# Kernel optimization log

Hardware: AMD Instinct MI355X
Metric: run time of the kernel (lower is better)

Reference implementation:

```python
import jax, jax.numpy as jnp
import numpy as np

N, D, K, R_DIM = 20000, 256, 16, 64
RADIUS = 50.0     # init radius
ALPHA = 2.0       # hardcoded in forward
THRESH = 0.01     # attention_threshold
EPS_LN = 1e-5     # torch LayerNorm default eps


def layer_norm(v, g, b):
    m = jnp.mean(v, axis=-1, keepdims=True)
    var = jnp.mean((v - m) ** 2, axis=-1, keepdims=True)
    return (v - m) / jnp.sqrt(var + EPS_LN) * g + b


def setup_inputs() -> dict:
    key = jax.random.key(0)
    ks = jax.random.split(key, 8)
    x = jax.random.normal(ks[0], (N, D), dtype=jnp.float32)
    # fixed-degree graph: node i has exactly K neighbors
    row = jnp.repeat(jnp.arange(N, dtype=jnp.int32), K)
    col = jax.random.randint(ks[1], (N * K,), 0, N, dtype=jnp.int32)
    edge_index = jnp.stack([row, col], axis=0)
    spatial_coords = jax.random.uniform(ks[2], (N, 2), dtype=jnp.float32) * 100.0
    gamma = jnp.ones((D,), jnp.float32)
    beta_ln = jnp.zeros((D,), jnp.float32)
    W_self = jax.random.normal(ks[3], (D, D), jnp.float32) * 0.05
    b_self = jnp.zeros((D,), jnp.float32)
    W_nei = jax.random.normal(ks[4], (D, D), jnp.float32) * 0.05
    b_nei = jnp.zeros((D,), jnp.float32)
    W_red = jax.random.normal(ks[5], (R_DIM, D), jnp.float32) * 0.05
    b_red = jnp.zeros((R_DIM,), jnp.float32)
    beta_mix = jnp.asarray(0.5, jnp.float32)
    return {"x": x, "spatial_coords": spatial_coords, "gamma": gamma,
            "beta_ln": beta_ln, "W_self": W_self, "b_self": b_self,
            "W_nei": W_nei, "b_nei": b_nei, "W_red": W_red, "b_red": b_red,
            "beta_mix": beta_mix, "edge_index": edge_index}


def reference(x, spatial_coords, gamma, beta_ln, W_self, b_self, W_nei, b_nei,
              W_red, b_red, beta_mix, edge_index):
    col = edge_index[1].reshape(N, K)              # fixed degree K per node
    neighbors = x[col]                             # [N, K, D] gather
    nb_coords = spatial_coords[col]                # [N, K, 2]
    distances = jnp.linalg.norm(spatial_coords[:, None, :] - nb_coords, axis=-1)  # [N, K]

    t = layer_norm(x, gamma, beta_ln)              # [N, D]
    nb = layer_norm(neighbors, gamma, beta_ln)     # [N, K, D]

    s_scores = t @ W_self.T + b_self               # [N, D]
    n_scores = nb @ W_nei.T + b_nei                # [N, K, D]

    dist_w = jnp.exp(-ALPHA * distances / (RADIUS + 1e-8))  # [N, K]
    weighted_n = n_scores * dist_w[..., None]

    combined = jnp.concatenate([s_scores[:, None, :], weighted_n], axis=1)  # [N, K+1, D]
    cw = jax.nn.softmax(combined, axis=1)
    self_w = cw[:, 0, :]
    nb_w = cw[:, 1:, :]
    self_w = jnp.where(jnp.abs(self_w) >= THRESH, self_w, 0.0)
    nb_w = jnp.where(jnp.abs(nb_w) >= THRESH, nb_w, 0.0)

    context = beta_mix * (self_w * t) + (1.0 - beta_mix) * jnp.sum(nb_w * nb, axis=1)
    reduced = jax.nn.leaky_relu(context @ W_red.T + b_red, 0.01)
    # outer forward applies leaky_relu again (dropout is identity in eval)
    return jax.nn.leaky_relu(reduced, 0.01)
```

## Files before the change

kernel.cpp:

```cpp
#include <hip/hip_runtime.h>
#include <cmath>

#define NN 20000
#define DD 256
#define KK 16
#define LDC3 768

typedef __attribute__((ext_vector_type(8))) short short8;
typedef __attribute__((ext_vector_type(4))) float f32x4;
typedef unsigned int u32;
typedef unsigned short bfu;

__device__ __forceinline__ float b2f(bfu u) {
  union { u32 i; float f; } v; v.i = ((u32)u) << 16; return v.f;
}
__device__ __forceinline__ bfu f2b(float f) {
  u32 u = __float_as_uint(f);
  u = (u + 0x7fff + ((u >> 16) & 1)) >> 16;
  return (bfu)u;
}
__device__ __forceinline__ float wave_sum(float v) {
#pragma unroll
  for (int m = 32; m; m >>= 1) v += __shfl_xor(v, m, 64);
  return v;
}
__device__ __forceinline__ void gl_lds16(const void* g, void* l) {
  __builtin_amdgcn_global_load_lds((const __attribute__((address_space(1))) u32*)g,
                                   (__attribute__((address_space(3))) u32*)l, 16, 0, 0);
}

__global__ __launch_bounds__(256) void prep_kernel(
    const float* __restrict__ x, const float* __restrict__ g,
    const float* __restrict__ b, const float* __restrict__ Wself,
    const float* __restrict__ Wnei, const float* __restrict__ Wred,
    bfu* __restrict__ C3, bfu* __restrict__ Wcat, bfu* __restrict__ Wredb) {
  int bid = blockIdx.x;
  if (bid < 5000) {
    int lane = threadIdx.x & 63;
    int row = (bid << 2) + (threadIdx.x >> 6);
    float4 v = ((const float4*)(x + (size_t)row * DD))[lane];
    float mean = wave_sum(v.x + v.y + v.z + v.w) * (1.0f / 256.0f);
    float4 d = make_float4(v.x - mean, v.y - mean, v.z - mean, v.w - mean);
    float var = wave_sum(d.x * d.x + d.y * d.y + d.z * d.z + d.w * d.w) * (1.0f / 256.0f);
    float rstd = 1.0f / sqrtf(var + 1e-5f);
    float4 g4 = ((const float4*)g)[lane];
    float4 b4 = ((const float4*)b)[lane];
    ushort4 ov;
    ov.x = f2b(d.x * rstd * g4.x + b4.x);
    ov.y = f2b(d.y * rstd * g4.y + b4.y);
    ov.z = f2b(d.z * rstd * g4.z + b4.z);
    ov.w = f2b(d.w * rstd * g4.w + b4.w);
    *(ushort4*)(C3 + (size_t)row * LDC3 + 512 + (lane << 2)) = ov;
  } else {
    int idx = (bid - 5000) * 256 + threadIdx.x;
    if (idx < 65536) Wcat[idx] = f2b(Wself[idx]);
    else if (idx < 131072) Wcat[idx] = f2b(Wnei[idx - 65536]);
    else if (idx < 147456) Wredb[idx - 131072] = f2b(Wred[idx - 131072]);
  }
}

template<int NT, bool FINAL>
__global__ __launch_bounds__(256) void gemm_kernel(
    const bfu* __restrict__ A, int lda, const bfu* __restrict__ Bw,
    const float* __restrict__ bias0, const float* __restrict__ bias1,
    void* __restrict__ Cout, int ldc, int M) {
  constexpr int FM = (NT == 128) ? 4 : 2;
  constexpr int WM = (NT == 128) ? 64 : 32;
  constexpr int AIT = 4;
  constexpr int BIT = NT / 32;
  __shared__ bfu smA[2][128 * 64];
  __shared__ bfu smB[2][NT * 64];
  int tid = threadIdx.x, lane = tid & 63, wid = tid >> 6;
  int m0 = blockIdx.x * 128;
  int nbase = blockIdx.y * NT;
  const bfu* Bt = Bw + (size_t)nbase * 256;
  int wr = (NT == 128) ? (wid >> 1) : wid;
  int wc = (NT == 128) ? (wid & 1) : 0;
  int lr = lane & 15, lk = lane >> 4;

  f32x4 acc[FM][4];
#pragma unroll
  for (int i = 0; i < FM; ++i)
#pragma unroll
    for (int j = 0; j < 4; ++j) acc[i][j] = (f32x4){0.f, 0.f, 0.f, 0.f};

#define STAGE(buf, kc)                                                          \
  {                                                                             \
    _Pragma("unroll") for (int i = 0; i < AIT; ++i) {                           \
      int p = tid + 256 * i; int row = p >> 3; int c = (p & 7) ^ (row & 7);     \
      gl_lds16(A + (size_t)(m0 + row) * lda + (kc) + c * 8, &smA[buf][p * 8]);  \
    }                                                                           \
    _Pragma("unroll") for (int i = 0; i < BIT; ++i) {                           \
      int p = tid + 256 * i; int row = p >> 3; int c = (p & 7) ^ (row & 7);     \
      gl_lds16(Bt + (size_t)row * 256 + (kc) + c * 8, &smB[buf][p * 8]);        \
    }                                                                           \
  }

#define COMPUTE(buf)                                                            \
  {                                                                             \
    _Pragma("unroll") for (int h = 0; h < 2; ++h) {                             \
      short8 af[FM], bfr[4];                                                    \
      int cc = h * 4 + lk;                                                      \
      _Pragma("unroll") for (int fm = 0; fm < FM; ++fm) {                       \
        int row = wr * WM + fm * 16 + lr;                                       \
        af[fm] = *(const short8*)&smA[buf][row * 64 + ((cc ^ (row & 7)) << 3)]; \
      }                                                                         \
      _Pragma("unroll") for (int fn = 0; fn < 4; ++fn) {                        \
        int row = wc * 64 + fn * 16 + lr;                                       \
        bfr[fn] = *(const short8*)&smB[buf][row * 64 + ((cc ^ (row & 7)) << 3)];\
      }                                                                         \
      _Pragma("unroll") for (int fm = 0; fm < FM; ++fm)                         \
        _Pragma("unroll") for (int fn = 0; fn < 4; ++fn)                        \
          acc[fm][fn] = __builtin_amdgcn_mfma_f32_16x16x32_bf16(                \
              bfr[fn], af[fm], acc[fm][fn], 0, 0, 0);                           \
    }                                                                           \
  }

  STAGE(0, 0);
  __syncthreads();
  STAGE(1, 64);
  COMPUTE(0);
  __syncthreads();
  STAGE(0, 128);
  COMPUTE(1);
  __syncthreads();
  STAGE(1, 192);
  COMPUTE(0);
  __syncthreads();
  COMPUTE(1);
#undef STAGE
#undef COMPUTE

  const float* bias = (nbase < 256) ? (bias0 + nbase) : (bias1 + (nbase - 256));
#pragma unroll
  for (int fm = 0; fm < FM; ++fm) {
    int m = m0 + wr * WM + fm * 16 + lr;
    if (m >= M) continue;
#pragma unroll
    for (int fn = 0; fn < 4; ++fn) {
      int lc = wc * 64 + fn * 16 + lk * 4;
      float4 bv = *(const float4*)(bias + lc);
      float o0 = acc[fm][fn][0] + bv.x;
      float o1 = acc[fm][fn][1] + bv.y;
      float o2 = acc[fm][fn][2] + bv.z;
      float o3 = acc[fm][fn][3] + bv.w;
      if (FINAL) {
        o0 = (o0 > 0.f) ? o0 : 0.01f * o0; o0 = (o0 > 0.f) ? o0 : 0.01f * o0;
        o1 = (o1 > 0.f) ? o1 : 0.01f * o1; o1 = (o1 > 0.f) ? o1 : 0.01f * o1;
        o2 = (o2 > 0.f) ? o2 : 0.01f * o2; o2 = (o2 > 0.f) ? o2 : 0.01f * o2;
        o3 = (o3 > 0.f) ? o3 : 0.01f * o3; o3 = (o3 > 0.f) ? o3 : 0.01f * o3;
        *(float4*)((float*)Cout + (size_t)m * ldc + nbase + lc) =
            make_float4(o0, o1, o2, o3);
      } else {
        ushort4 ov; ov.x = f2b(o0); ov.y = f2b(o1); ov.z = f2b(o2); ov.w = f2b(o3);
        *(ushort4*)((bfu*)Cout + (size_t)m * ldc + nbase + lc) = ov;
      }
    }
  }
}

__global__ __launch_bounds__(256) void gather_kernel(
    const bfu* __restrict__ C3, const float* __restrict__ coords,
    const int* __restrict__ col, const float* __restrict__ bmix,
    bfu* __restrict__ ctx) {
  const float L2E = 1.4426950408889634f;
  int lane = threadIdx.x & 63;
  int i = (blockIdx.x << 2) + (threadIdx.x >> 6);
  float beta = bmix[0];

  int ck = col[i * KK + (lane & 15)];
  float2 ci = ((const float2*)coords)[i];
  float2 cn = ((const float2*)coords)[ck];
  float dx = ci.x - cn.x, dy = ci.y - cn.y;
  float dwv = exp2f((-2.0f * L2E / (50.0f + 1e-8f)) * sqrtf(dx * dx + dy * dy)) * L2E;

  int d = lane << 2;
  const bfu* rowi = C3 + (size_t)i * LDC3;
  ushort4 sv = *(const ushort4*)(rowi + d);
  float4 e0 = make_float4(exp2f(L2E * b2f(sv.x)), exp2f(L2E * b2f(sv.y)),
                          exp2f(L2E * b2f(sv.z)), exp2f(L2E * b2f(sv.w)));
  float4 Z = e0;
  float4 ef[KK];
  ushort4 tn[KK];
#pragma unroll
  for (int k = 0; k < KK; ++k) {
    int cc = __shfl(ck, k, 64);
    float w = __shfl(dwv, k, 64);
    const bfu* rowc = C3 + (size_t)cc * LDC3;
    ushort4 uv = *(const ushort4*)(rowc + 256 + d);
    tn[k] = *(const ushort4*)(rowc + 512 + d);
    float4 e = make_float4(exp2f(w * b2f(uv.x)), exp2f(w * b2f(uv.y)),
                           exp2f(w * b2f(uv.z)), exp2f(w * b2f(uv.w)));
    ef[k] = e;
    Z.x += e.x; Z.y += e.y; Z.z += e.z; Z.w += e.w;
  }
  float4 thr = make_float4(0.01f * Z.x, 0.01f * Z.y, 0.01f * Z.z, 0.01f * Z.w);
  ushort4 tv = *(const ushort4*)(rowi + 512 + d);
  float ob = 1.0f - beta;
  float4 ns = make_float4(0.f, 0.f, 0.f, 0.f);
#pragma unroll
  for (int k = 0; k < KK; ++k) {
    float ex = (ef[k].x >= thr.x) ? ef[k].x : 0.f;
    float ey = (ef[k].y >= thr.y) ? ef[k].y : 0.f;
    float ez = (ef[k].z >= thr.z) ? ef[k].z : 0.f;
    float ew = (ef[k].w >= thr.w) ? ef[k].w : 0.f;
    ns.x += ex * b2f(tn[k].x); ns.y += ey * b2f(tn[k].y);
    ns.z += ez * b2f(tn[k].z); ns.w += ew * b2f(tn[k].w);
  }
  float s0x = (e0.x >= thr.x) ? e0.x : 0.f;
  float s0y = (e0.y >= thr.y) ? e0.y : 0.f;
  float s0z = (e0.z >= thr.z) ? e0.z : 0.f;
  float s0w = (e0.w >= thr.w) ? e0.w : 0.f;
  ushort4 ov;
  ov.x = f2b((beta * s0x * b2f(tv.x) + ob * ns.x) / Z.x);
  ov.y = f2b((beta * s0y * b2f(tv.y) + ob * ns.y) / Z.y);
  ov.z = f2b((beta * s0z * b2f(tv.z) + ob * ns.z) / Z.z);
  ov.w = f2b((beta * s0w * b2f(tv.w) + ob * ns.w) / Z.w);
  *(ushort4*)(ctx + (size_t)i * DD + d) = ov;
}

extern "C" void kernel_launch(void* const* d_in, const int* in_sizes, int n_in,
                              void* d_out, int out_size, void* d_ws, size_t ws_size,
                              hipStream_t stream) {
  (void)in_sizes; (void)n_in; (void)out_size; (void)ws_size;
  const float* x       = (const float*)d_in[0];
  const float* coords  = (const float*)d_in[1];
  const float* gamma   = (const float*)d_in[2];
  const float* beta_ln = (const float*)d_in[3];
  const float* W_self  = (const float*)d_in[4];
  const float* b_self  = (const float*)d_in[5];
  const float* W_nei   = (const float*)d_in[6];
  const float* b_nei   = (const float*)d_in[7];
  const float* W_red   = (const float*)d_in[8];
  const float* b_red   = (const float*)d_in[9];
  const float* bmix    = (const float*)d_in[10];
  const int*   edge    = (const int*)d_in[11];
  const int*   col     = edge + (size_t)NN * KK;

  bfu* C3    = (bfu*)d_ws;
  bfu* ctx   = (bfu*)((char*)d_ws + 30867456);
  bfu* Wcat  = (bfu*)((char*)d_ws + 41156608);
  bfu* Wredb = (bfu*)((char*)d_ws + 41418752);

  prep_kernel<<<5577, 256, 0, stream>>>(x, gamma, beta_ln, W_self, W_nei, W_red,
                                        C3, Wcat, Wredb);
  gemm_kernel<128, false><<<dim3(157, 4), 256, 0, stream>>>(
      C3 + 512, LDC3, Wcat, b_self, b_nei, (void*)C3, LDC3, NN);
  gather_kernel<<<5000, 256, 0, stream>>>(C3, coords, col, bmix, ctx);
  gemm_kernel<64, true><<<dim3(157, 1), 256, 0, stream>>>(
      ctx, DD, Wredb, b_red, b_red, d_out, 64, NN);
}
```

Measured before the change: 159.8 us.

## Interleave neighbor scores with normalized features and tighten GEMM pipeline waits

Widens the workspace row to 1024 bf16 and interleaves each 4-element chunk of neighbor scores with the matching 4 layer-normed values. The gather kernel can then fetch both with a single 16-byte load per neighbor instead of two 8-byte loads from separate regions. The GEMM prefetches two stages up front and uses explicit vmcnt waits with raw barriers instead of __syncthreads, so loads overlap compute. The final GEMM switches to 64x64 tiles, doubling the grid to 313 blocks, at the cost of an extra LN copy write and a larger workspace.

```diff
diff --git a/kernel.cpp b/kernel.cpp
--- a/kernel.cpp
+++ b/kernel.cpp
@@ -4,7 +4,7 @@
 #define NN 20000
 #define DD 256
 #define KK 16
-#define LDC3 768
+#define LDROW 1024
 
 typedef __attribute__((ext_vector_type(8))) short short8;
 typedef __attribute__((ext_vector_type(4))) float f32x4;
@@ -27,6 +27,14 @@
 __device__ __forceinline__ void gl_lds16(const void* g, void* l) {
   __builtin_amdgcn_global_load_lds((const __attribute__((address_space(1))) u32*)g,
                                    (__attribute__((address_space(3))) u32*)l, 16, 0, 0);
+}
+template<int N> __device__ __forceinline__ void wait_vm() {
+  asm volatile("s_waitcnt vmcnt(%0)" :: "i"(N) : "memory");
+}
+__device__ __forceinline__ void bar() {
+  __builtin_amdgcn_sched_barrier(0);
+  __builtin_amdgcn_s_barrier();
+  __builtin_amdgcn_sched_barrier(0);
 }
 
 __global__ __launch_bounds__(256) void prep_kernel(
@@ -50,7 +58,9 @@
     ov.y = f2b(d.y * rstd * g4.y + b4.y);
     ov.z = f2b(d.z * rstd * g4.z + b4.z);
     ov.w = f2b(d.w * rstd * g4.w + b4.w);
-    *(ushort4*)(C3 + (size_t)row * LDC3 + 512 + (lane << 2)) = ov;
+    bfu* rowp = C3 + (size_t)row * LDROW;
+    *(ushort4*)(rowp + 768 + (lane << 2)) = ov;
+    *(ushort4*)(rowp + 256 + (lane << 3) + 4) = ov;
   } else {
     int idx = (bid - 5000) * 256 + threadIdx.x;
     if (idx < 65536) Wcat[idx] = f2b(Wself[idx]);
@@ -59,36 +69,34 @@
   }
 }
 
-template<int NT, bool FINAL>
+template<int MT, int NT, int LDA, bool FINAL>
 __global__ __launch_bounds__(256) void gemm_kernel(
-    const bfu* __restrict__ A, int lda, const bfu* __restrict__ Bw,
+    const bfu* __restrict__ A, const bfu* __restrict__ Bw,
     const float* __restrict__ bias0, const float* __restrict__ bias1,
-    void* __restrict__ Cout, int ldc, int M) {
-  constexpr int FM = (NT == 128) ? 4 : 2;
-  constexpr int WM = (NT == 128) ? 64 : 32;
-  constexpr int AIT = 4;
-  constexpr int BIT = NT / 32;
-  __shared__ bfu smA[2][128 * 64];
+    bfu* __restrict__ C3out, float* __restrict__ Fout, int M) {
+  constexpr int WM = MT / 2, WN = NT / 2, FM = WM / 16, FN = WN / 16;
+  constexpr int AIT = MT * 8 / 256, BIT = NT * 8 / 256;
+  constexpr int VM = (MT + NT) / 32;
+  __shared__ bfu smA[2][MT * 64];
   __shared__ bfu smB[2][NT * 64];
   int tid = threadIdx.x, lane = tid & 63, wid = tid >> 6;
-  int m0 = blockIdx.x * 128;
+  int m0 = blockIdx.x * MT;
   int nbase = blockIdx.y * NT;
   const bfu* Bt = Bw + (size_t)nbase * 256;
-  int wr = (NT == 128) ? (wid >> 1) : wid;
-  int wc = (NT == 128) ? (wid & 1) : 0;
+  int wr = wid >> 1, wc = wid & 1;
   int lr = lane & 15, lk = lane >> 4;
 
-  f32x4 acc[FM][4];
+  f32x4 acc[FM][FN];
 #pragma unroll
   for (int i = 0; i < FM; ++i)
 #pragma unroll
-    for (int j = 0; j < 4; ++j) acc[i][j] = (f32x4){0.f, 0.f, 0.f, 0.f};
+    for (int j = 0; j < FN; ++j) acc[i][j] = (f32x4){0.f, 0.f, 0.f, 0.f};
 
 #define STAGE(buf, kc)                                                          \
   {                                                                             \
     _Pragma("unroll") for (int i = 0; i < AIT; ++i) {                           \
       int p = tid + 256 * i; int row = p >> 3; int c = (p & 7) ^ (row & 7);     \
-      gl_lds16(A + (size_t)(m0 + row) * lda + (kc) + c * 8, &smA[buf][p * 8]);  \
+      gl_lds16(A + (size_t)(m0 + row) * LDA + (kc) + c * 8, &smA[buf][p * 8]);  \
     }                                                                           \
     _Pragma("unroll") for (int i = 0; i < BIT; ++i) {                           \
       int p = tid + 256 * i; int row = p >> 3; int c = (p & 7) ^ (row & 7);     \
@@ -99,34 +107,36 @@
 #define COMPUTE(buf)                                                            \
   {                                                                             \
     _Pragma("unroll") for (int h = 0; h < 2; ++h) {                             \
-      short8 af[FM], bfr[4];                                                    \
+      short8 af[FM], bfr[FN];                                                   \
       int cc = h * 4 + lk;                                                      \
       _Pragma("unroll") for (int fm = 0; fm < FM; ++fm) {                       \
         int row = wr * WM + fm * 16 + lr;                                       \
         af[fm] = *(const short8*)&smA[buf][row * 64 + ((cc ^ (row & 7)) << 3)]; \
       }                                                                         \
-      _Pragma("unroll") for (int fn = 0; fn < 4; ++fn) {                        \
-        int row = wc * 64 + fn * 16 + lr;                                       \
+      _Pragma("unroll") for (int fn = 0; fn < FN; ++fn) {                       \
+        int row = wc * WN + fn * 16 + lr;                                       \
         bfr[fn] = *(const short8*)&smB[buf][row * 64 + ((cc ^ (row & 7)) << 3)];\
       }                                                                         \
       _Pragma("unroll") for (int fm = 0; fm < FM; ++fm)                         \
-        _Pragma("unroll") for (int fn = 0; fn < 4; ++fn)                        \
+        _Pragma("unroll") for (int fn = 0; fn < FN; ++fn)                       \
           acc[fm][fn] = __builtin_amdgcn_mfma_f32_16x16x32_bf16(                \
               bfr[fn], af[fm], acc[fm][fn], 0, 0, 0);                           \
     }                                                                           \
   }
 
   STAGE(0, 0);
-  __syncthreads();
   STAGE(1, 64);
+  wait_vm<VM>(); bar();
   COMPUTE(0);
-  __syncthreads();
+  bar();
   STAGE(0, 128);
+  wait_vm<VM>(); bar();
   COMPUTE(1);
-  __syncthreads();
+  bar();
   STAGE(1, 192);
+  wait_vm<VM>(); bar();
   COMPUTE(0);
-  __syncthreads();
+  wait_vm<0>(); bar();
   COMPUTE(1);
 #undef STAGE
 #undef COMPUTE
@@ -137,8 +147,8 @@
     int m = m0 + wr * WM + fm * 16 + lr;
     if (m >= M) continue;
 #pragma unroll
-    for (int fn = 0; fn < 4; ++fn) {
-      int lc = wc * 64 + fn * 16 + lk * 4;
+    for (int fn = 0; fn < FN; ++fn) {
+      int lc = wc * WN + fn * 16 + lk * 4;
       float4 bv = *(const float4*)(bias + lc);
       float o0 = acc[fm][fn][0] + bv.x;
       float o1 = acc[fm][fn][1] + bv.y;
@@ -149,11 +159,15 @@
         o1 = (o1 > 0.f) ? o1 : 0.01f * o1; o1 = (o1 > 0.f) ? o1 : 0.01f * o1;
         o2 = (o2 > 0.f) ? o2 : 0.01f * o2; o2 = (o2 > 0.f) ? o2 : 0.01f * o2;
         o3 = (o3 > 0.f) ? o3 : 0.01f * o3; o3 = (o3 > 0.f) ? o3 : 0.01f * o3;
-        *(float4*)((float*)Cout + (size_t)m * ldc + nbase + lc) =
-            make_float4(o0, o1, o2, o3);
+        *(float4*)(Fout + (size_t)m * NT + nbase + lc) = make_float4(o0, o1, o2, o3);
       } else {
         ushort4 ov; ov.x = f2b(o0); ov.y = f2b(o1); ov.z = f2b(o2); ov.w = f2b(o3);
-        *(ushort4*)((bfu*)Cout + (size_t)m * ldc + nbase + lc) = ov;
+        if (nbase < 256) {
+          *(ushort4*)(C3out + (size_t)m * LDROW + nbase + lc) = ov;
+        } else {
+          int f = nbase - 256 + lc;
+          *(ushort4*)(C3out + (size_t)m * LDROW + 256 + ((f >> 2) << 3)) = ov;
+        }
       }
     }
   }
@@ -175,8 +189,9 @@
   float dwv = exp2f((-2.0f * L2E / (50.0f + 1e-8f)) * sqrtf(dx * dx + dy * dy)) * L2E;
 
   int d = lane << 2;
-  const bfu* rowi = C3 + (size_t)i * LDC3;
+  const bfu* rowi = C3 + (size_t)i * LDROW;
   ushort4 sv = *(const ushort4*)(rowi + d);
+  short8 self8 = *(const short8*)(rowi + 256 + (lane << 3));
   float4 e0 = make_float4(exp2f(L2E * b2f(sv.x)), exp2f(L2E * b2f(sv.y)),
                           exp2f(L2E * b2f(sv.z)), exp2f(L2E * b2f(sv.w)));
   float4 Z = e0;
@@ -186,16 +201,14 @@
   for (int k = 0; k < KK; ++k) {
     int cc = __shfl(ck, k, 64);
     float w = __shfl(dwv, k, 64);
-    const bfu* rowc = C3 + (size_t)cc * LDC3;
-    ushort4 uv = *(const ushort4*)(rowc + 256 + d);
-    tn[k] = *(const ushort4*)(rowc + 512 + d);
-    float4 e = make_float4(exp2f(w * b2f(uv.x)), exp2f(w * b2f(uv.y)),
-                           exp2f(w * b2f(uv.z)), exp2f(w * b2f(uv.w)));
+    short8 v = *(const short8*)(C3 + (size_t)cc * LDROW + 256 + (lane << 3));
+    tn[k].x = (bfu)v[4]; tn[k].y = (bfu)v[5]; tn[k].z = (bfu)v[6]; tn[k].w = (bfu)v[7];
+    float4 e = make_float4(exp2f(w * b2f((bfu)v[0])), exp2f(w * b2f((bfu)v[1])),
+                           exp2f(w * b2f((bfu)v[2])), exp2f(w * b2f((bfu)v[3])));
     ef[k] = e;
     Z.x += e.x; Z.y += e.y; Z.z += e.z; Z.w += e.w;
   }
   float4 thr = make_float4(0.01f * Z.x, 0.01f * Z.y, 0.01f * Z.z, 0.01f * Z.w);
-  ushort4 tv = *(const ushort4*)(rowi + 512 + d);
   float ob = 1.0f - beta;
   float4 ns = make_float4(0.f, 0.f, 0.f, 0.f);
 #pragma unroll
@@ -212,10 +225,10 @@
   float s0z = (e0.z >= thr.z) ? e0.z : 0.f;
   float s0w = (e0.w >= thr.w) ? e0.w : 0.f;
   ushort4 ov;
-  ov.x = f2b((beta * s0x * b2f(tv.x) + ob * ns.x) / Z.x);
-  ov.y = f2b((beta * s0y * b2f(tv.y) + ob * ns.y) / Z.y);
-  ov.z = f2b((beta * s0z * b2f(tv.z) + ob * ns.z) / Z.z);
-  ov.w = f2b((beta * s0w * b2f(tv.w) + ob * ns.w) / Z.w);
+  ov.x = f2b((beta * s0x * b2f((bfu)self8[4]) + ob * ns.x) / Z.x);
+  ov.y = f2b((beta * s0y * b2f((bfu)self8[5]) + ob * ns.y) / Z.y);
+  ov.z = f2b((beta * s0z * b2f((bfu)self8[6]) + ob * ns.z) / Z.z);
+  ov.w = f2b((beta * s0w * b2f((bfu)self8[7]) + ob * ns.w) / Z.w);
   *(ushort4*)(ctx + (size_t)i * DD + d) = ov;
 }
 
@@ -238,15 +251,15 @@
   const int*   col     = edge + (size_t)NN * KK;
 
   bfu* C3    = (bfu*)d_ws;
-  bfu* ctx   = (bfu*)((char*)d_ws + 30867456);
-  bfu* Wcat  = (bfu*)((char*)d_ws + 41156608);
-  bfu* Wredb = (bfu*)((char*)d_ws + 41418752);
-
-  prep_kernel<<<5577, 256, 0, stream>>>(x, gamma, beta_ln, W_self, W_nei, W_red,
+  bfu* ctx   = (bfu*)((char*)d_ws + 41156608);
+  bfu* Wcat  = (bfu*)((char*)d_ws + 51445760);
+  bfu* Wredb = (bfu*)((char*)d_ws + 51707904);
+
+  prep_kernel<<<5576, 256, 0, stream>>>(x, gamma, beta_ln, W_self, W_nei, W_red,
                                         C3, Wcat, Wredb);
-  gemm_kernel<128, false><<<dim3(157, 4), 256, 0, stream>>>(
-      C3 + 512, LDC3, Wcat, b_self, b_nei, (void*)C3, LDC3, NN);
+  gemm_kernel<128, 128, LDROW, false><<<dim3(157, 4), 256, 0, stream>>>(
+      C3 + 768, Wcat, b_self, b_nei, C3, nullptr, NN);
   gather_kernel<<<5000, 256, 0, stream>>>(C3, coords, col, bmix, ctx);
-  gemm_kernel<64, true><<<dim3(157, 1), 256, 0, stream>>>(
-      ctx, DD, Wredb, b_red, b_red, d_out, 64, NN);
-}
+  gemm_kernel<64, 64, 256, true><<<dim3(313, 1), 256, 0, stream>>>(
+      ctx, Wredb, b_red, b_red, nullptr, (float*)d_out, NN);
+}
```

After: 173.6 us. 1.09x slower.

## Fuse final reduction GEMM into gather kernel and use fast exp2/rcp

Applied to the files above, without the earlier changes.

The final 256->64 projection and double leaky_relu are folded into the gather kernel. Each block stages its 4 context rows in LDS as bf16 and runs a 16x16x32 MFMA per wave against bf16 W_red, writing fp32 output directly. This removes the ctx round trip through global memory and one kernel launch, and the GEMM kernel loses its template. The cost is 12 of 16 MFMA rows doing wasted work on uninitialized LDS, plus an added __syncthreads. exp2f and the division are also swapped for the hardware exp2 and rcp intrinsics, which trades a little precision for fewer instructions.

```diff
diff --git a/kernel.cpp b/kernel.cpp
--- a/kernel.cpp
+++ b/kernel.cpp
@@ -28,6 +28,8 @@
   __builtin_amdgcn_global_load_lds((const __attribute__((address_space(1))) u32*)g,
                                    (__attribute__((address_space(3))) u32*)l, 16, 0, 0);
 }
+__device__ __forceinline__ float fexp2(float x) { return __builtin_amdgcn_exp2f(x); }
+__device__ __forceinline__ float frcp(float x)  { return __builtin_amdgcn_rcpf(x); }
 
 __global__ __launch_bounds__(256) void prep_kernel(
     const float* __restrict__ x, const float* __restrict__ g,
@@ -59,61 +61,55 @@
   }
 }
 
-template<int NT, bool FINAL>
 __global__ __launch_bounds__(256) void gemm_kernel(
-    const bfu* __restrict__ A, int lda, const bfu* __restrict__ Bw,
+    const bfu* __restrict__ A, const bfu* __restrict__ Bw,
     const float* __restrict__ bias0, const float* __restrict__ bias1,
-    void* __restrict__ Cout, int ldc, int M) {
-  constexpr int FM = (NT == 128) ? 4 : 2;
-  constexpr int WM = (NT == 128) ? 64 : 32;
-  constexpr int AIT = 4;
-  constexpr int BIT = NT / 32;
+    bfu* __restrict__ Cout, int M) {
   __shared__ bfu smA[2][128 * 64];
-  __shared__ bfu smB[2][NT * 64];
+  __shared__ bfu smB[2][128 * 64];
   int tid = threadIdx.x, lane = tid & 63, wid = tid >> 6;
   int m0 = blockIdx.x * 128;
-  int nbase = blockIdx.y * NT;
+  int nbase = blockIdx.y * 128;
   const bfu* Bt = Bw + (size_t)nbase * 256;
-  int wr = (NT == 128) ? (wid >> 1) : wid;
-  int wc = (NT == 128) ? (wid & 1) : 0;
+  int wr = wid >> 1, wc = wid & 1;
   int lr = lane & 15, lk = lane >> 4;
 
-  f32x4 acc[FM][4];
-#pragma unroll
-  for (int i = 0; i < FM; ++i)
+  f32x4 acc[4][4];
+#pragma unroll
+  for (int i = 0; i < 4; ++i)
 #pragma unroll
     for (int j = 0; j < 4; ++j) acc[i][j] = (f32x4){0.f, 0.f, 0.f, 0.f};
 
-#define STAGE(buf, kc)                                                          \
-  {                                                                             \
-    _Pragma("unroll") for (int i = 0; i < AIT; ++i) {                           \
-      int p = tid + 256 * i; int row = p >> 3; int c = (p & 7) ^ (row & 7);     \
-      gl_lds16(A + (size_t)(m0 + row) * lda + (kc) + c * 8, &smA[buf][p * 8]);  \
-    }                                                                           \
-    _Pragma("unroll") for (int i = 0; i < BIT; ++i) {                           \
-      int p = tid + 256 * i; int row = p >> 3; int c = (p & 7) ^ (row & 7);     \
-      gl_lds16(Bt + (size_t)row * 256 + (kc) + c * 8, &smB[buf][p * 8]);        \
-    }                                                                           \
-  }
-
-#define COMPUTE(buf)                                                            \
-  {                                                                             \
-    _Pragma("unroll") for (int h = 0; h < 2; ++h) {                             \
-      short8 af[FM], bfr[4];                                                    \
-      int cc = h * 4 + lk;                                                      \
-      _Pragma("unroll") for (int fm = 0; fm < FM; ++fm) {                       \
-        int row = wr * WM + fm * 16 + lr;                                       \
-        af[fm] = *(const short8*)&smA[buf][row * 64 + ((cc ^ (row & 7)) << 3)]; \
-      }                                                                         \
-      _Pragma("unroll") for (int fn = 0; fn < 4; ++fn) {                        \
-        int row = wc * 64 + fn * 16 + lr;                                       \
-        bfr[fn] = *(const short8*)&smB[buf][row * 64 + ((cc ^ (row & 7)) << 3)];\
-      }                                                                         \
-      _Pragma("unroll") for (int fm = 0; fm < FM; ++fm)                         \
-        _Pragma("unroll") for (int fn = 0; fn < 4; ++fn)                        \
-          acc[fm][fn] = __builtin_amdgcn_mfma_f32_16x16x32_bf16(                \
-              bfr[fn], af[fm], acc[fm][fn], 0, 0, 0);                           \
-    }                                                                           \
+#define STAGE(buf, kc)                                                           \
+  {                                                                              \
+    _Pragma("unroll") for (int i = 0; i < 4; ++i) {                              \
+      int p = tid + 256 * i; int row = p >> 3; int c = (p & 7) ^ (row & 7);      \
+      gl_lds16(A + (size_t)(m0 + row) * LDC3 + (kc) + c * 8, &smA[buf][p * 8]);  \
+    }                                                                            \
+    _Pragma("unroll") for (int i = 0; i < 4; ++i) {                              \
+      int p = tid + 256 * i; int row = p >> 3; int c = (p & 7) ^ (row & 7);      \
+      gl_lds16(Bt + (size_t)row * 256 + (kc) + c * 8, &smB[buf][p * 8]);         \
+    }                                                                            \
+  }
+
+#define COMPUTE(buf)                                                             \
+  {                                                                              \
+    _Pragma("unroll") for (int h = 0; h < 2; ++h) {                              \
+      short8 af[4], bfr[4];                                                      \
+      int cc = h * 4 + lk;                                                       \
+      _Pragma("unroll") for (int fm = 0; fm < 4; ++fm) {                         \
+        int row = wr * 64 + fm * 16 + lr;                                        \
+        af[fm] = *(const short8*)&smA[buf][row * 64 + ((cc ^ (row & 7)) << 3)];  \
+      }                                                                          \
+      _Pragma("unroll") for (int fn = 0; fn < 4; ++fn) {                         \
+        int row = wc * 64 + fn * 16 + lr;                                        \
+        bfr[fn] = *(const short8*)&smB[buf][row * 64 + ((cc ^ (row & 7)) << 3)]; \
+      }                                                                          \
+      _Pragma("unroll") for (int fm = 0; fm < 4; ++fm)                           \
+        _Pragma("unroll") for (int fn = 0; fn < 4; ++fn)                         \
+          acc[fm][fn] = __builtin_amdgcn_mfma_f32_16x16x32_bf16(                 \
+              bfr[fn], af[fm], acc[fm][fn], 0, 0, 0);                            \
+    }                                                                            \
   }
 
   STAGE(0, 0);
@@ -133,28 +129,19 @@
 
   const float* bias = (nbase < 256) ? (bias0 + nbase) : (bias1 + (nbase - 256));
 #pragma unroll
-  for (int fm = 0; fm < FM; ++fm) {
-    int m = m0 + wr * WM + fm * 16 + lr;
+  for (int fm = 0; fm < 4; ++fm) {
+    int m = m0 + wr * 64 + fm * 16 + lr;
     if (m >= M) continue;
 #pragma unroll
     for (int fn = 0; fn < 4; ++fn) {
       int lc = wc * 64 + fn * 16 + lk * 4;
       float4 bv = *(const float4*)(bias + lc);
-      float o0 = acc[fm][fn][0] + bv.x;
-      float o1 = acc[fm][fn][1] + bv.y;
-      float o2 = acc[fm][fn][2] + bv.z;
-      float o3 = acc[fm][fn][3] + bv.w;
-      if (FINAL) {
-        o0 = (o0 > 0.f) ? o0 : 0.01f * o0; o0 = (o0 > 0.f) ? o0 : 0.01f * o0;
-        o1 = (o1 > 0.f) ? o1 : 0.01f * o1; o1 = (o1 > 0.f) ? o1 : 0.01f * o1;
-        o2 = (o2 > 0.f) ? o2 : 0.01f * o2; o2 = (o2 > 0.f) ? o2 : 0.01f * o2;
-        o3 = (o3 > 0.f) ? o3 : 0.01f * o3; o3 = (o3 > 0.f) ? o3 : 0.01f * o3;
-        *(float4*)((float*)Cout + (size_t)m * ldc + nbase + lc) =
-            make_float4(o0, o1, o2, o3);
-      } else {
-        ushort4 ov; ov.x = f2b(o0); ov.y = f2b(o1); ov.z = f2b(o2); ov.w = f2b(o3);
-        *(ushort4*)((bfu*)Cout + (size_t)m * ldc + nbase + lc) = ov;
-      }
+      ushort4 ov;
+      ov.x = f2b(acc[fm][fn][0] + bv.x);
+      ov.y = f2b(acc[fm][fn][1] + bv.y);
+      ov.z = f2b(acc[fm][fn][2] + bv.z);
+      ov.w = f2b(acc[fm][fn][3] + bv.w);
+      *(ushort4*)(Cout + (size_t)m * LDC3 + nbase + lc) = ov;
     }
   }
 }
@@ -162,35 +149,39 @@
 __global__ __launch_bounds__(256) void gather_kernel(
     const bfu* __restrict__ C3, const float* __restrict__ coords,
     const int* __restrict__ col, const float* __restrict__ bmix,
-    bfu* __restrict__ ctx) {
+    const bfu* __restrict__ Wred, const float* __restrict__ bred,
+    float* __restrict__ out) {
+  __shared__ bfu cstage[16][264];
   const float L2E = 1.4426950408889634f;
   int lane = threadIdx.x & 63;
-  int i = (blockIdx.x << 2) + (threadIdx.x >> 6);
+  int w = threadIdx.x >> 6;
+  int i0 = blockIdx.x << 2;
+  int i = i0 + w;
   float beta = bmix[0];
 
   int ck = col[i * KK + (lane & 15)];
   float2 ci = ((const float2*)coords)[i];
   float2 cn = ((const float2*)coords)[ck];
   float dx = ci.x - cn.x, dy = ci.y - cn.y;
-  float dwv = exp2f((-2.0f * L2E / (50.0f + 1e-8f)) * sqrtf(dx * dx + dy * dy)) * L2E;
+  float dwv = fexp2((-2.0f * L2E / (50.0f + 1e-8f)) * sqrtf(dx * dx + dy * dy)) * L2E;
 
   int d = lane << 2;
   const bfu* rowi = C3 + (size_t)i * LDC3;
   ushort4 sv = *(const ushort4*)(rowi + d);
-  float4 e0 = make_float4(exp2f(L2E * b2f(sv.x)), exp2f(L2E * b2f(sv.y)),
-                          exp2f(L2E * b2f(sv.z)), exp2f(L2E * b2f(sv.w)));
+  float4 e0 = make_float4(fexp2(L2E * b2f(sv.x)), fexp2(L2E * b2f(sv.y)),
+                          fexp2(L2E * b2f(sv.z)), fexp2(L2E * b2f(sv.w)));
   float4 Z = e0;
   float4 ef[KK];
   ushort4 tn[KK];
 #pragma unroll
   for (int k = 0; k < KK; ++k) {
     int cc = __shfl(ck, k, 64);
-    float w = __shfl(dwv, k, 64);
+    float ww = __shfl(dwv, k, 64);
     const bfu* rowc = C3 + (size_t)cc * LDC3;
     ushort4 uv = *(const ushort4*)(rowc + 256 + d);
     tn[k] = *(const ushort4*)(rowc + 512 + d);
-    float4 e = make_float4(exp2f(w * b2f(uv.x)), exp2f(w * b2f(uv.y)),
-                           exp2f(w * b2f(uv.z)), exp2f(w * b2f(uv.w)));
+    float4 e = make_float4(fexp2(ww * b2f(uv.x)), fexp2(ww * b2f(uv.y)),
+                           fexp2(ww * b2f(uv.z)), fexp2(ww * b2f(uv.w)));
     ef[k] = e;
     Z.x += e.x; Z.y += e.y; Z.z += e.z; Z.w += e.w;
   }
@@ -211,12 +202,34 @@
   float s0y = (e0.y >= thr.y) ? e0.y : 0.f;
   float s0z = (e0.z >= thr.z) ? e0.z : 0.f;
   float s0w = (e0.w >= thr.w) ? e0.w : 0.f;
-  ushort4 ov;
-  ov.x = f2b((beta * s0x * b2f(tv.x) + ob * ns.x) / Z.x);
-  ov.y = f2b((beta * s0y * b2f(tv.y) + ob * ns.y) / Z.y);
-  ov.z = f2b((beta * s0z * b2f(tv.z) + ob * ns.z) / Z.z);
-  ov.w = f2b((beta * s0w * b2f(tv.w) + ob * ns.w) / Z.w);
-  *(ushort4*)(ctx + (size_t)i * DD + d) = ov;
+  float4 iz = make_float4(frcp(Z.x), frcp(Z.y), frcp(Z.z), frcp(Z.w));
+  ushort4 cb;
+  cb.x = f2b((beta * s0x * b2f(tv.x) + ob * ns.x) * iz.x);
+  cb.y = f2b((beta * s0y * b2f(tv.y) + ob * ns.y) * iz.y);
+  cb.z = f2b((beta * s0z * b2f(tv.z) + ob * ns.z) * iz.z);
+  cb.w = f2b((beta * s0w * b2f(tv.w) + ob * ns.w) * iz.w);
+  *(ushort4*)&cstage[w][d] = cb;
+  __syncthreads();
+
+  int lr16 = lane & 15, lk4 = lane >> 4;
+  const bfu* wrow = Wred + (size_t)(w * 16 + lr16) * 256 + (lk4 << 3);
+  f32x4 racc = (f32x4){0.f, 0.f, 0.f, 0.f};
+#pragma unroll
+  for (int ks = 0; ks < 8; ++ks) {
+    short8 av = *(const short8*)&cstage[lr16][ks * 32 + (lk4 << 3)];
+    short8 bv = *(const short8*)(wrow + ks * 32);
+    racc = __builtin_amdgcn_mfma_f32_16x16x32_bf16(av, bv, racc, 0, 0, 0);
+  }
+  if (lane < 16) {
+    float bb = bred[w * 16 + lane];
+#pragma unroll
+    for (int q = 0; q < 4; ++q) {
+      float vv = racc[q] + bb;
+      vv = (vv > 0.f) ? vv : 0.01f * vv;
+      vv = (vv > 0.f) ? vv : 0.01f * vv;
+      out[(size_t)(i0 + q) * 64 + w * 16 + lane] = vv;
+    }
+  }
 }
 
 extern "C" void kernel_launch(void* const* d_in, const int* in_sizes, int n_in,
@@ -238,15 +251,13 @@
   const int*   col     = edge + (size_t)NN * KK;
 
   bfu* C3    = (bfu*)d_ws;
-  bfu* ctx   = (bfu*)((char*)d_ws + 30867456);
-  bfu* Wcat  = (bfu*)((char*)d_ws + 41156608);
-  bfu* Wredb = (bfu*)((char*)d_ws + 41418752);
-
-  prep_kernel<<<5577, 256, 0, stream>>>(x, gamma, beta_ln, W_self, W_nei, W_red,
+  bfu* Wcat  = (bfu*)((char*)d_ws + 30867456);
+  bfu* Wredb = (bfu*)((char*)d_ws + 31129600);
+
+  prep_kernel<<<5576, 256, 0, stream>>>(x, gamma, beta_ln, W_self, W_nei, W_red,
                                         C3, Wcat, Wredb);
-  gemm_kernel<128, false><<<dim3(157, 4), 256, 0, stream>>>(
-      C3 + 512, LDC3, Wcat, b_self, b_nei, (void*)C3, LDC3, NN);
-  gather_kernel<<<5000, 256, 0, stream>>>(C3, coords, col, bmix, ctx);
-  gemm_kernel<64, true><<<dim3(157, 1), 256, 0, stream>>>(
-      ctx, DD, Wredb, b_red, b_red, d_out, 64, NN);
-}
+  gemm_kernel<<<dim3(157, 4), 256, 0, stream>>>(
+      C3 + 512, Wcat, b_self, b_nei, C3, NN);
+  gather_kernel<<<5000, 256, 0, stream>>>(C3, coords, col, bmix, Wredb, b_red,
+                                          (float*)d_out);
+}
```

New measurement: 160.9 us. About the same (+0.6%).
